# Performance work log

Measured on AMD Instinct MI355X. Metric: run time of the kernel, lower is better.

## Reference

```python
import jax, jax.numpy as jnp
import numpy as np

V = 50000      # vocab_size
E = 512        # embed_size
H = 512        # hidden_size
B = 128        # batch
S = 256        # encoder seq len
MAX_OOVS = 12


def setup_inputs() -> dict:
    key = jax.random.key(0)
    ks = jax.random.split(key, 18)
    s = 0.05
    embed_table = jax.random.normal(ks[4], (V, E), jnp.float32) * s
    embed_table = embed_table.at[0].set(0.0)  # padding_idx=0
    return {
        'input_idx':   jax.random.randint(ks[0], (B,), 0, V),
        'encoded':     jax.random.normal(ks[1], (B, S, H), jnp.float32),
        'encoded_idx': jax.random.randint(ks[2], (B, S), 0, V),
        'prev_state':  jax.random.normal(ks[3], (B, H), jnp.float32),
        'weighted':    jnp.zeros((B, 1, H), jnp.float32),
        'embed_table': embed_table,
        'Ws_w':    jax.random.normal(ks[5], (H, H), jnp.float32) * s,
        'Ws_b':    jnp.zeros((H,), jnp.float32),
        'gru_Wih': jax.random.normal(ks[6], (3 * H, E + H), jnp.float32) * s,
        'gru_Whh': jax.random.normal(ks[7], (3 * H, H), jnp.float32) * s,
        'gru_bih': jnp.zeros((3 * H,), jnp.float32),
        'gru_bhh': jnp.zeros((3 * H,), jnp.float32),
        'attn_W':  jax.random.normal(ks[8], (H, 2 * H), jnp.float32) * s,
        'attn_b':  jnp.zeros((H,), jnp.float32),
        'attn_v':  jax.random.normal(ks[9], (H,), jnp.float32) * s,
        'Wo_w':    jax.random.normal(ks[10], (V, 2 * H), jnp.float32) * s,
        'Wo_b':    jnp.zeros((V,), jnp.float32),
        'Wc_w':    jax.random.normal(ks[11], (2 * H, H), jnp.float32) * s,
        'Wc_b':    jnp.zeros((2 * H,), jnp.float32),
    }


def copy_decoder_fwd(input_idx, encoded, encoded_idx, prev_state, weighted,
                     embed_table, Ws_w, Ws_b, gru_Wih, gru_Whh, gru_bih, gru_bhh,
                     attn_W, attn_b, attn_v, Wo_w, Wo_b, Wc_w, Wc_b):
    b, seq, hidden = encoded.shape
    vocab = Wo_w.shape[0]
    dt = encoded.dtype

    # order == 0 branch: project prev_state, zero the weighted context
    prev = prev_state @ Ws_w.T + Ws_b                      # (b, h)
    wtd = jnp.zeros((b, hidden), dt)                       # (b, h)

    # GRU single step (PyTorch gate layout: r, z, n)
    x = jnp.concatenate([embed_table[input_idx], wtd], axis=1)  # (b, e+h)
    gi = x @ gru_Wih.T + gru_bih                           # (b, 3h)
    gh = prev @ gru_Whh.T + gru_bhh                        # (b, 3h)
    i_r, i_z, i_n = jnp.split(gi, 3, axis=1)
    h_r, h_z, h_n = jnp.split(gh, 3, axis=1)
    r = jax.nn.sigmoid(i_r + h_r)
    z = jax.nn.sigmoid(i_z + h_z)
    n = jnp.tanh(i_n + r * h_n)
    state = (1.0 - z) * n + z * prev                       # (b, h), == rnn_output

    # 'concat' attention: softmax_seq(v . tanh(W[h; enc] + b))
    h_exp = jnp.broadcast_to(state[:, None, :], (b, seq, hidden))
    energy = jnp.tanh(jnp.concatenate([h_exp, encoded], axis=-1) @ attn_W.T + attn_b)
    attn_w = jax.nn.softmax(energy @ attn_v, axis=1)       # (b, seq)
    context = jnp.einsum('bs,bsh->bh', attn_w, encoded)    # (b, h)

    # generation scores
    score_g = jnp.concatenate([state, context], axis=1) @ Wo_w.T + Wo_b  # (b, V)

    # copy scores
    sc = jnp.tanh(encoded @ Wc_w.T + Wc_b)                 # (b, seq, 2h)
    score_c = jnp.einsum('bsk,bk->bs', sc, jnp.concatenate([state, context], axis=1))
    score_c = score_c + jnp.where(encoded_idx == 0, -1000.0, 0.0).astype(dt)

    # joint softmax over vocab + seq
    probs = jax.nn.softmax(jnp.concatenate([score_g, score_c], axis=1), axis=1)
    prob_g = probs[:, :vocab]                              # (b, V)
    prob_c = probs[:, vocab:]                              # (b, seq)
    prob_c_given = prob_c / jnp.sum(prob_c)                # global-scalar normalization (faithful)

    # pad generation probs with small oov mass
    vext = vocab + MAX_OOVS
    prob_g_ext = jnp.concatenate(
        [prob_g, jnp.full((b, MAX_OOVS), 1e-4, dt)], axis=1)  # (b, V+oov)

    # copy -> vocab scatter-add (replaces dense one-hot + bmm)
    batch_ids = jnp.broadcast_to(jnp.arange(b)[:, None], (b, seq))
    prob_c_to_g = jnp.zeros((b, vext), dt).at[batch_ids, encoded_idx].add(prob_c)

    out = (prob_g_ext + prob_c_to_g)[:, None, :]           # (b, 1, V+oov)

    # positions in source equal to the current input token
    ind = (encoded_idx == input_idx[:, None]).astype(dt)   # (b, seq)
    ssum = ind.sum(axis=1, keepdims=True)
    ind = jnp.where(ssum > 1.0, ind / ssum, ind)
    attn2 = prob_c_given * ind                             # (b, seq)
    weighted_new = jnp.einsum('bs,bsh->bh', attn2, encoded)[:, None, :]  # (b, 1, h)

    return out, state, weighted_new


def reference(input_idx, encoded, encoded_idx, prev_state, weighted,
              embed_table, Ws_w, Ws_b, gru_Wih, gru_Whh, gru_bih, gru_bhh,
              attn_W, attn_b, attn_v, Wo_w, Wo_b, Wc_w, Wc_b):
    return copy_decoder_fwd(input_idx, encoded, encoded_idx, prev_state, weighted,
                            embed_table, Ws_w, Ws_b, gru_Wih, gru_Whh, gru_bih, gru_bhh,
                            attn_W, attn_b, attn_v, Wo_w, Wo_b, Wc_w, Wc_b)
```

## Files before the change

kernel.cpp:

```cpp
#include <hip/hip_runtime.h>
#include <hip/hip_bf16.h>
#include <math.h>

#define BB 128
#define SS 256
#define HH 512
#define VV 50000
#define VEXT 50012
#define NBLK 782
#define PST 784

typedef __bf16 bf16x8 __attribute__((ext_vector_type(8)));
typedef float f32x4 __attribute__((ext_vector_type(4)));

__device__ __forceinline__ float fast_tanh(float x) {
  float e = __expf(2.0f * x);
  return 1.0f - 2.0f / (e + 1.0f);
}
__device__ __forceinline__ float fast_sigmoid(float x) {
  return 1.0f / (1.0f + __expf(-x));
}
__device__ __forceinline__ bf16x8 cvt8(const float* p) {
  float4 a = *(const float4*)p;
  float4 b = *(const float4*)(p + 4);
  bf16x8 r;
  r[0] = (__bf16)a.x; r[1] = (__bf16)a.y; r[2] = (__bf16)a.z; r[3] = (__bf16)a.w;
  r[4] = (__bf16)b.x; r[5] = (__bf16)b.y; r[6] = (__bf16)b.z; r[7] = (__bf16)b.w;
  return r;
}

__device__ __forceinline__ void gload_lds16(const bf16x8* g, bf16x8* l) {
  __builtin_amdgcn_global_load_lds((const __attribute__((address_space(1))) void*)g,
                                   (__attribute__((address_space(3))) void*)l, 16, 0, 0);
}

__global__ void k_pack_all(const float* __restrict__ Wc_w, const float* __restrict__ attn_W,
                           const float* __restrict__ enc,
                           __hip_bfloat16* __restrict__ wc_bf,
                           __hip_bfloat16* __restrict__ wa_bf,
                           __hip_bfloat16* __restrict__ epk,
                           float* __restrict__ pc_total) {
  int i = blockIdx.x * 256 + threadIdx.x;
  if (blockIdx.x == 0 && threadIdx.x == 0) pc_total[0] = 0.f;
  if (i < 65536) {
    int l = i & 63, ks = (i >> 6) & 15, tile = i >> 10;
    int m = l & 15, q = l >> 4;
    const float* p = Wc_w + (size_t)(tile * 16 + m) * 512 + ks * 32 + q * 8;
    *(bf16x8*)(wc_bf + (size_t)i * 8) = cvt8(p);
  } else if (i < 98304) {
    int j = i - 65536;
    int l = j & 63, ks = (j >> 6) & 15, tile = j >> 10;
    int m = l & 15, q = l >> 4;
    const float* p = attn_W + (size_t)(tile * 16 + m) * 1024 + 512 + ks * 32 + q * 8;
    *(bf16x8*)(wa_bf + (size_t)j * 8) = cvt8(p);
  } else if (i < 98304 + 2097152) {
    int j = i - 98304;
    int l = j & 63, ks = (j >> 6) & 15, st = (j >> 10) & 15, b = j >> 14;
    int m = l & 15, q = l >> 4;
    const float* p = enc + ((size_t)b * SS + st * 16 + m) * HH + ks * 32 + q * 8;
    *(bf16x8*)(epk + (size_t)j * 8) = cvt8(p);
  }
}

template <int LDB, bool GATHER>
__global__ __launch_bounds__(256, 2) void k_gemm_bt(
    const float* __restrict__ A, const float* __restrict__ B,
    const float* __restrict__ bias, float* __restrict__ C, int ldc,
    const int* __restrict__ gidx) {
  __shared__ __hip_bfloat16 ylds[128 * 72];
  const int t = threadIdx.x;
  const int l = t & 63, w = t >> 6;
  const int m = l & 15, q = l >> 4;
  const int n = blockIdx.x * 64 + w * 16 + m;
  const float* wrow = B + (size_t)n * LDB;
  f32x4 acc[8];
#pragma unroll
  for (int mt = 0; mt < 8; ++mt) acc[mt] = (f32x4){0.f, 0.f, 0.f, 0.f};

  for (int kt = 0; kt < 512; kt += 64) {
    __syncthreads();
#pragma unroll
    for (int i = 0; i < 8; ++i) {
      int f = t + i * 256;
      int row = f >> 4, c4 = f & 15;
      const float* arow;
      if (GATHER)
        arow = A + (size_t)gidx[row] * 512;
      else
        arow = A + (size_t)row * 512;
      float4 v = *(const float4*)(arow + kt + c4 * 4);
      __hip_bfloat16* d = ylds + row * 72 + c4 * 4;
      d[0] = __float2bfloat16(v.x); d[1] = __float2bfloat16(v.y);
      d[2] = __float2bfloat16(v.z); d[3] = __float2bfloat16(v.w);
    }
    __syncthreads();
#pragma unroll
    for (int ksl = 0; ksl < 2; ++ksl) {
      bf16x8 bfr = cvt8(wrow + kt + ksl * 32 + q * 8);
#pragma unroll
      for (int mt = 0; mt < 8; ++mt) {
        bf16x8 af = *(const bf16x8*)(ylds + (mt * 16 + m) * 72 + ksl * 32 + q * 8);
        acc[mt] = __builtin_amdgcn_mfma_f32_16x16x32_bf16(af, bfr, acc[mt], 0, 0, 0);
      }
    }
  }
  float bv = bias[n];
#pragma unroll
  for (int mt = 0; mt < 8; ++mt) {
#pragma unroll
    for (int r = 0; r < 4; ++r) {
      int rowm = mt * 16 + q * 4 + r;
      C[(size_t)rowm * ldc + n] = acc[mt][r] + bv;
    }
  }
}

__global__ __launch_bounds__(256, 2) void k_gemm_dual(
    const float* __restrict__ A0, const float* __restrict__ B0,
    const float* __restrict__ b0, float* __restrict__ C0, int ldb0, int ldc0, int nb0,
    const float* __restrict__ A1, const float* __restrict__ B1,
    const float* __restrict__ b1, float* __restrict__ C1, int ldb1, int ldc1,
    const int* __restrict__ gidx1) {
  __shared__ __hip_bfloat16 ylds[128 * 72];
  const float* A; const float* Bw; const float* bias; float* C;
  int ldb, ldc, blk; const int* gidx;
  if ((int)blockIdx.x < nb0) {
    A = A0; Bw = B0; bias = b0; C = C0; ldb = ldb0; ldc = ldc0; gidx = nullptr; blk = blockIdx.x;
  } else {
    A = A1; Bw = B1; bias = b1; C = C1; ldb = ldb1; ldc = ldc1; gidx = gidx1; blk = blockIdx.x - nb0;
  }
  const int t = threadIdx.x;
  const int l = t & 63, w = t >> 6;
  const int m = l & 15, q = l >> 4;
  const int n = blk * 64 + w * 16 + m;
  const float* wrow = Bw + (size_t)n * ldb;
  f32x4 acc[8];
#pragma unroll
  for (int mt = 0; mt < 8; ++mt) acc[mt] = (f32x4){0.f, 0.f, 0.f, 0.f};

  for (int kt = 0; kt < 512; kt += 64) {
    __syncthreads();
#pragma unroll
    for (int i = 0; i < 8; ++i) {
      int f = t + i * 256;
      int row = f >> 4, c4 = f & 15;
      const float* arow = gidx ? (A + (size_t)gidx[row] * 512) : (A + (size_t)row * 512);
      float4 v = *(const float4*)(arow + kt + c4 * 4);
      __hip_bfloat16* d = ylds + row * 72 + c4 * 4;
      d[0] = __float2bfloat16(v.x); d[1] = __float2bfloat16(v.y);
      d[2] = __float2bfloat16(v.z); d[3] = __float2bfloat16(v.w);
    }
    __syncthreads();
#pragma unroll
    for (int ksl = 0; ksl < 2; ++ksl) {
      bf16x8 bfr = cvt8(wrow + kt + ksl * 32 + q * 8);
#pragma unroll
      for (int mt = 0; mt < 8; ++mt) {
        bf16x8 af = *(const bf16x8*)(ylds + (mt * 16 + m) * 72 + ksl * 32 + q * 8);
        acc[mt] = __builtin_amdgcn_mfma_f32_16x16x32_bf16(af, bfr, acc[mt], 0, 0, 0);
      }
    }
  }
  float bv = bias[n];
#pragma unroll
  for (int mt = 0; mt < 8; ++mt) {
#pragma unroll
    for (int r = 0; r < 4; ++r) {
      int rowm = mt * 16 + q * 4 + r;
      C[(size_t)rowm * ldc + n] = acc[mt][r] + bv;
    }
  }
}

__global__ void k_gates(const float* __restrict__ gi, const float* __restrict__ gh,
                        const float* __restrict__ prevv, float* __restrict__ state,
                        float* __restrict__ state_out) {
  int i = blockIdx.x * 256 + threadIdx.x;
  int b = i >> 9, h = i & 511;
  const float* gib = gi + (size_t)b * 1536;
  const float* ghb = gh + (size_t)b * 1536;
  float ir = gib[h], iz = gib[512 + h], inn = gib[1024 + h];
  float hr = ghb[h], hz = ghb[512 + h], hn = ghb[1024 + h];
  float r = fast_sigmoid(ir + hr);
  float z = fast_sigmoid(iz + hz);
  float n = fast_tanh(inn + r * hn);
  float st = (1.f - z) * n + z * prevv[i];
  state[i] = st;
  state_out[i] = st;
}

template <int NTOT, int MODE>
__global__ __launch_bounds__(256, 2) void k_fused3(
    const __hip_bfloat16* __restrict__ epack, const __hip_bfloat16* __restrict__ wpk,
    const float* __restrict__ biasA, const float* __restrict__ multA,
    const int* __restrict__ enc_idx, float* __restrict__ out) {
  const int b = blockIdx.x, t = threadIdx.x;
  const int l = t & 63, w = t >> 6;
  const int m = l & 15, q = l >> 4;
  const int st = blockIdx.y * 4 + w;
  __shared__ bf16x8 wbuf[2][2048];
  __shared__ float bias_l[NTOT];
  __shared__ float mult_l[NTOT];
  const float* bias_base = (MODE == 0) ? biasA + (size_t)b * HH : biasA;
  const float* mult_base = (MODE == 0) ? multA : multA + (size_t)b * 1024;
  for (int i = t; i < NTOT; i += 256) {
    bias_l[i] = bias_base[i];
    mult_l[i] = mult_base[i];
  }
  const __hip_bfloat16* ep = epack + ((size_t)(b * 16 + st) * 16) * 512 + (size_t)l * 8;
  bf16x8 afr[16];
#pragma unroll
  for (int ks = 0; ks < 16; ++ks) afr[ks] = *(const bf16x8*)(ep + ks * 512);

  const bf16x8* wv = (const bf16x8*)wpk;
  constexpr int NITER = NTOT / 32;
#pragma unroll
  for (int i = 0; i < 8; ++i)
    gload_lds16(wv + w * 64 + i * 256 + l, &wbuf[0][w * 64 + i * 256]);
  __syncthreads();

  float part[4] = {0.f, 0.f, 0.f, 0.f};
  int cur = 0;
  for (int it = 0; it < NITER; ++it) {
    if (it + 1 < NITER) {
      const bf16x8* src = wv + (size_t)(it + 1) * 2048;
#pragma unroll
      for (int i = 0; i < 8; ++i)
        gload_lds16(src + w * 64 + i * 256 + l, &wbuf[cur ^ 1][w * 64 + i * 256]);
    }
    const int nb = it * 32;
#pragma unroll
    for (int nt = 0; nt < 2; ++nt) {
      const __hip_bfloat16* wbase = (const __hip_bfloat16*)&wbuf[cur][0] + nt * 8192 + (size_t)l * 8;
      f32x4 a0 = {0.f, 0.f, 0.f, 0.f}, a1 = a0, a2 = a0, a3 = a0;
#pragma unroll
      for (int j = 0; j < 4; ++j) {
        a0 = __builtin_amdgcn_mfma_f32_16x16x32_bf16(afr[j], *(const bf16x8*)(wbase + j * 512), a0, 0, 0, 0);
        a1 = __builtin_amdgcn_mfma_f32_16x16x32_bf16(afr[4 + j], *(const bf16x8*)(wbase + (4 + j) * 512), a1, 0, 0, 0);
        a2 = __builtin_amdgcn_mfma_f32_16x16x32_bf16(afr[8 + j], *(const bf16x8*)(wbase + (8 + j) * 512), a2, 0, 0, 0);
        a3 = __builtin_amdgcn_mfma_f32_16x16x32_bf16(afr[12 + j], *(const bf16x8*)(wbase + (12 + j) * 512), a3, 0, 0, 0);
      }
      f32x4 acc = (a0 + a1) + (a2 + a3);
      const int n = nb + nt * 16 + m;
      float bias = bias_l[n];
      float mul = mult_l[n];
#pragma unroll
      for (int r = 0; r < 4; ++r) part[r] += fast_tanh(acc[r] + bias) * mul;
    }
    __syncthreads();
    cur ^= 1;
  }
#pragma unroll
  for (int r = 0; r < 4; ++r) {
    part[r] += __shfl_xor(part[r], 1, 64);
    part[r] += __shfl_xor(part[r], 2, 64);
    part[r] += __shfl_xor(part[r], 4, 64);
    part[r] += __shfl_xor(part[r], 8, 64);
  }
  if (m == 0) {
#pragma unroll
    for (int r = 0; r < 4; ++r) {
      int s = st * 16 + q * 4 + r;
      float v = part[r];
      if (MODE == 1 && enc_idx[b * SS + s] == 0) v -= 1000.0f;
      out[b * SS + s] = v;
    }
  }
}

__global__ __launch_bounds__(256, 4) void k_score_g2(
    const __hip_bfloat16* __restrict__ ypk, const float* __restrict__ Wo_w,
    const float* __restrict__ Wo_b, float* __restrict__ sg,
    float* __restrict__ ppmax, float* __restrict__ ppsum) {
  const int t = threadIdx.x;
  const int l = t & 63, w = t >> 6;
  const int m = l & 15, q = l >> 4;
  const int blk = blockIdx.x;
  const int n = blk * 64 + w * 16 + m;
  const int n_ld = (n < VV) ? n : (VV - 1);
  const float* wrow = Wo_w + (size_t)n_ld * 1024;
  f32x4 acc[8];
#pragma unroll
  for (int mt = 0; mt < 8; ++mt) acc[mt] = (f32x4){0.f, 0.f, 0.f, 0.f};

  for (int ks = 0; ks < 32; ++ks) {
    bf16x8 bfr = cvt8(wrow + ks * 32 + q * 8);
#pragma unroll
    for (int mt = 0; mt < 8; ++mt) {
      bf16x8 af = *(const bf16x8*)(ypk + (((size_t)mt * 32 + ks) * 64 + l) * 8);
      acc[mt] = __builtin_amdgcn_mfma_f32_16x16x32_bf16(af, bfr, acc[mt], 0, 0, 0);
    }
  }

  float bv = (n < VV) ? Wo_b[n] : 0.f;
#pragma unroll
  for (int mt = 0; mt < 8; ++mt) {
#pragma unroll
    for (int r = 0; r < 4; ++r) {
      float v = acc[mt][r] + bv;
      if (n < VV)
        sg[(size_t)(mt * 16 + q * 4 + r) * VV + n] = v;
      else
        v = -1e30f;
      acc[mt][r] = v;
    }
  }

  __shared__ float redA[4][128];
  __shared__ float MS[128];
#pragma unroll
  for (int mt = 0; mt < 8; ++mt) {
#pragma unroll
    for (int r = 0; r < 4; ++r) {
      float mx = acc[mt][r];
      mx = fmaxf(mx, __shfl_xor(mx, 1, 64));
      mx = fmaxf(mx, __shfl_xor(mx, 2, 64));
      mx = fmaxf(mx, __shfl_xor(mx, 4, 64));
      mx = fmaxf(mx, __shfl_xor(mx, 8, 64));
      if (m == 0) redA[w][mt * 16 + q * 4 + r] = mx;
    }
  }
  __syncthreads();
  if (t < 128)
    MS[t] = fmaxf(fmaxf(redA[0][t], redA[1][t]), fmaxf(redA[2][t], redA[3][t]));
  __syncthreads();
#pragma unroll
  for (int mt = 0; mt < 8; ++mt) {
#pragma unroll
    for (int r = 0; r < 4; ++r) {
      float s = __expf(acc[mt][r] - MS[mt * 16 + q * 4 + r]);
      s += __shfl_xor(s, 1, 64);
      s += __shfl_xor(s, 2, 64);
      s += __shfl_xor(s, 4, 64);
      s += __shfl_xor(s, 8, 64);
      if (m == 0) redA[w][mt * 16 + q * 4 + r] = s;
    }
  }
  __syncthreads();
  if (t < 128) {
    ppmax[(size_t)t * PST + blk] = MS[t];
    ppsum[(size_t)t * PST + blk] = redA[0][t] + redA[1][t] + redA[2][t] + redA[3][t];
  }
}

__global__ void k_merge(const float* __restrict__ ppmax, const float* __restrict__ ppsum,
                        const float* __restrict__ sc,
                        float* __restrict__ rmax, float* __restrict__ rsum,
                        float* __restrict__ prob_c, float* __restrict__ pc_total) {
  const int row = blockIdx.x, t = threadIdx.x;
  __shared__ float rb[8];
  __shared__ float MS[2];
  float x_sc = sc[row * SS + t];
  float mrow = x_sc;
  for (int i = t; i < NBLK; i += 256) mrow = fmaxf(mrow, ppmax[(size_t)row * PST + i]);
  for (int off = 32; off > 0; off >>= 1) mrow = fmaxf(mrow, __shfl_xor(mrow, off, 64));
  if ((t & 63) == 0) rb[t >> 6] = mrow;
  __syncthreads();
  if (t == 0) MS[0] = fmaxf(fmaxf(rb[0], rb[1]), fmaxf(rb[2], rb[3]));
  __syncthreads();
  float M = MS[0];
  float e_sc = __expf(x_sc - M);
  float s = e_sc;
  for (int i = t; i < NBLK; i += 256)
    s += ppsum[(size_t)row * PST + i] * __expf(ppmax[(size_t)row * PST + i] - M);
  for (int off = 32; off > 0; off >>= 1) s += __shfl_xor(s, off, 64);
  if ((t & 63) == 0) rb[4 + (t >> 6)] = s;
  __syncthreads();
  if (t == 0) MS[1] = rb[4] + rb[5] + rb[6] + rb[7];
  __syncthreads();
  float S = MS[1];
  if (t == 0) {
    rmax[row] = M;
    rsum[row] = S;
  }
  float pc = e_sc / S;
  prob_c[row * SS + t] = pc;
  float ps = pc;
  for (int off = 32; off > 0; off >>= 1) ps += __shfl_xor(ps, off, 64);
  if ((t & 63) == 0) rb[t >> 6] = ps;
  __syncthreads();
  if (t == 0) atomicAdd(pc_total, rb[0] + rb[1] + rb[2] + rb[3]);
}

__global__ void k_ctx(const float* __restrict__ score, const float* __restrict__ enc,
                      const float* __restrict__ state, float* __restrict__ y,
                      __hip_bfloat16* __restrict__ ypk) {
  const int b = blockIdx.x, hc = blockIdx.y, t = threadIdx.x;
  __shared__ float aws[SS];
  __shared__ float rb[4];
  float x0 = score[b * SS + t], x1 = score[b * SS + t + 128];
  float mx = fmaxf(x0, x1);
  for (int off = 32; off > 0; off >>= 1) mx = fmaxf(mx, __shfl_xor(mx, off, 64));
  if ((t & 63) == 0) rb[t >> 6] = mx;
  __syncthreads();
  mx = fmaxf(rb[0], rb[1]);
  float e0 = __expf(x0 - mx), e1 = __expf(x1 - mx);
  float s = e0 + e1;
  for (int off = 32; off > 0; off >>= 1) s += __shfl_xor(s, off, 64);
  if ((t & 63) == 0) rb[2 + (t >> 6)] = s;
  __syncthreads();
  float inv = 1.0f / (rb[2] + rb[3]);
  aws[t] = e0 * inv;
  aws[t + 128] = e1 * inv;
  __syncthreads();
  const int h = hc * 128 + t;
  float acc = 0.f;
#pragma unroll 8
  for (int ss = 0; ss < SS; ++ss) acc += aws[ss] * enc[((size_t)b * SS + ss) * HH + h];
  float sv = state[b * HH + h];
  y[(size_t)b * 1024 + h] = sv;
  y[(size_t)b * 1024 + HH + h] = acc;
  const int tile = b >> 4, mm = b & 15;
  const int c0 = h, c1 = HH + h;
  ypk[(((size_t)tile * 32 + (c0 >> 5)) * 64 + ((c0 & 31) >> 3) * 16 + mm) * 8 + (c0 & 7)] =
      __float2bfloat16(sv);
  ypk[(((size_t)tile * 32 + (c1 >> 5)) * 64 + ((c1 & 31) >> 3) * 16 + mm) * 8 + (c1 & 7)] =
      __float2bfloat16(acc);
}

__global__ void k_write_probg(const float* __restrict__ sg,
                              const float* __restrict__ rmax,
                              const float* __restrict__ rsum,
                              float* __restrict__ out) {
  int i = blockIdx.x * 256 + threadIdx.x;
  const int total = BB * VEXT;
  if (i >= total) return;
  int b = i / VEXT;
  int v = i - b * VEXT;
  float val;
  if (v < VV)
    val = __expf(sg[(size_t)b * VV + v] - rmax[b]) / rsum[b];
  else
    val = 1e-4f;
  out[i] = val;
}

__global__ void k_weighted2(const int* __restrict__ enc_idx,
                            const int* __restrict__ input_idx,
                            const float* __restrict__ prob_c,
                            const float* __restrict__ pc_total,
                            const float* __restrict__ enc,
                            float* __restrict__ wout,
                            float* __restrict__ out) {
  const int b = blockIdx.x, hc = blockIdx.y, t = threadIdx.x;
  __shared__ float f[SS];
  __shared__ float rb[2];
  const int idx_in = input_idx[b];
  const int e0i = enc_idx[b * SS + t], e1i = enc_idx[b * SS + t + 128];
  const float p0 = prob_c[b * SS + t], p1 = prob_c[b * SS + t + 128];
  if (hc == 0) {
    atomicAdd(&out[(size_t)b * VEXT + e0i], p0);
    atomicAdd(&out[(size_t)b * VEXT + e1i], p1);
  }
  int m0 = (e0i == idx_in) ? 1 : 0;
  int m1 = (e1i == idx_in) ? 1 : 0;
  float lsum = (float)(m0 + m1);
  for (int off = 32; off > 0; off >>= 1) lsum += __shfl_xor(lsum, off, 64);
  if ((t & 63) == 0) rb[t >> 6] = lsum;
  __syncthreads();
  float tot = rb[0] + rb[1];
  float norm = (tot > 1.0f) ? 1.0f / tot : 1.0f;
  float inv_pct = 1.0f / pc_total[0];
  f[t] = m0 ? p0 * inv_pct * norm : 0.f;
  f[t + 128] = m1 ? p1 * inv_pct * norm : 0.f;
  __syncthreads();
  const int h = hc * 128 + t;
  float acc = 0.f;
  for (int ss = 0; ss < SS; ++ss) acc += f[ss] * enc[((size_t)b * SS + ss) * HH + h];
  wout[b * HH + h] = acc;
}

extern "C" void kernel_launch(void* const* d_in, const int* in_sizes, int n_in,
                              void* d_out, int out_size, void* d_ws, size_t ws_size,
                              hipStream_t stream) {
  const int* input_idx = (const int*)d_in[0];
  const float* encoded = (const float*)d_in[1];
  const int* encoded_idx = (const int*)d_in[2];
  const float* prev_state = (const float*)d_in[3];
  const float* embed = (const float*)d_in[5];
  const float* Ws_w = (const float*)d_in[6];
  const float* Ws_b = (const float*)d_in[7];
  const float* gWih = (const float*)d_in[8];
  const float* gWhh = (const float*)d_in[9];
  const float* gbih = (const float*)d_in[10];
  const float* gbhh = (const float*)d_in[11];
  const float* attn_W = (const float*)d_in[12];
  const float* attn_b = (const float*)d_in[13];
  const float* attn_v = (const float*)d_in[14];
  const float* Wo_w = (const float*)d_in[15];
  const float* Wo_b = (const float*)d_in[16];
  const float* Wc_w = (const float*)d_in[17];
  const float* Wc_b = (const float*)d_in[18];

  float* out = (float*)d_out;
  float* out_state = out + (size_t)BB * VEXT;
  float* out_weighted = out_state + BB * HH;

  float* ws = (float*)d_ws;
  float* prevv = ws;
  float* state = prevv + BB * HH;
  float* hW = state + BB * HH;
  float* ascore = hW + BB * HH;
  float* aw = ascore + BB * SS;
  float* y = aw + BB * SS;
  float* sg = y + BB * 1024;
  float* sc = sg + (size_t)BB * VV;
  float* prob_c = sc + BB * SS;
  float* rmax = prob_c + BB * SS;
  float* rsum = rmax + BB;
  float* pc_total = rsum + BB;
  float* ppmax = pc_total + 64;
  float* ppsum = ppmax + (size_t)BB * PST;
  __hip_bfloat16* wc_bf = (__hip_bfloat16*)(ppsum + (size_t)BB * PST);
  __hip_bfloat16* wa_bf = wc_bf + (size_t)1024 * HH;
  __hip_bfloat16* epack = wa_bf + (size_t)512 * HH;
  __hip_bfloat16* ypk = epack + (size_t)BB * SS * HH;

  float* gi = sg;
  float* gh = sg + BB * 1536;

  k_pack_all<<<8576, 256, 0, stream>>>(Wc_w, attn_W, encoded, wc_bf, wa_bf, epack, pc_total);

  k_gemm_dual<<<32, 256, 0, stream>>>(prev_state, Ws_w, Ws_b, prevv, 512, 512, 8,
                                      embed, gWih, gbih, gi, 1024, 1536, input_idx);
  k_gemm_bt<512, false><<<24, 256, 0, stream>>>(prevv, gWhh, gbhh, gh, 1536, nullptr);
  k_gates<<<256, 256, 0, stream>>>(gi, gh, prevv, state, out_state);
  k_gemm_bt<1024, false><<<8, 256, 0, stream>>>(state, attn_W, attn_b, hW, 512, nullptr);

  k_fused3<HH, 0><<<dim3(BB, 4), 256, 0, stream>>>(epack, wa_bf, hW, attn_v,
                                                   nullptr, ascore);
  k_ctx<<<dim3(BB, 4), 128, 0, stream>>>(ascore, encoded, state, y, ypk);

  k_score_g2<<<NBLK, 256, 0, stream>>>(ypk, Wo_w, Wo_b, sg, ppmax, ppsum);
  k_fused3<1024, 1><<<dim3(BB, 4), 256, 0, stream>>>(epack, wc_bf, Wc_b, y,
                                                     encoded_idx, sc);

  k_merge<<<BB, 256, 0, stream>>>(ppmax, ppsum, sc, rmax, rsum, prob_c, pc_total);
  k_write_probg<<<(BB * VEXT + 255) / 256, 256, 0, stream>>>(sg, rmax, rsum, out);
  k_weighted2<<<dim3(BB, 4), 128, 0, stream>>>(encoded_idx, input_idx, prob_c, pc_total,
                                               encoded, out_weighted, out);
}
```

Baseline: 697.3 us.

## Split vocab-score GEMM tiles across batch halves and prefetch weight fragments

The output-projection kernel now covers 32 vocab columns per block instead of 64. Its four waves are split into two column tiles by two batch halves, so each wave keeps four accumulators instead of eight, and the launch bound allows eight blocks per CU. The kernel launches twice as many blocks, and the next k-step's Wo_w fragment is loaded while the current MFMAs run. The cost is that each weight row is now read by two waves. The partial max/sum buffers double in size, so the merge kernel reads more entries per row.

```diff
diff --git a/kernel.cpp b/kernel.cpp
--- a/kernel.cpp
+++ b/kernel.cpp
@@ -7,8 +7,8 @@
 #define HH 512
 #define VV 50000
 #define VEXT 50012
-#define NBLK 782
-#define PST 784
+#define NBLK2 1563
+#define PST 1568
 
 typedef __bf16 bf16x8 __attribute__((ext_vector_type(8)));
 typedef float f32x4 __attribute__((ext_vector_type(4)));
@@ -268,48 +268,53 @@
   }
 }
 
-__global__ __launch_bounds__(256, 4) void k_score_g2(
+__global__ __launch_bounds__(256, 8) void k_score_g3(
     const __hip_bfloat16* __restrict__ ypk, const float* __restrict__ Wo_w,
     const float* __restrict__ Wo_b, float* __restrict__ sg,
     float* __restrict__ ppmax, float* __restrict__ ppsum) {
   const int t = threadIdx.x;
   const int l = t & 63, w = t >> 6;
   const int m = l & 15, q = l >> 4;
+  const int ntile = w & 1, mhalf = w >> 1;
   const int blk = blockIdx.x;
-  const int n = blk * 64 + w * 16 + m;
+  const int n = blk * 32 + ntile * 16 + m;
   const int n_ld = (n < VV) ? n : (VV - 1);
   const float* wrow = Wo_w + (size_t)n_ld * 1024;
-  f32x4 acc[8];
-#pragma unroll
-  for (int mt = 0; mt < 8; ++mt) acc[mt] = (f32x4){0.f, 0.f, 0.f, 0.f};
-
+  const __hip_bfloat16* ybase = ypk + ((size_t)mhalf * 4 * 32 * 64 + l) * 8;
+  f32x4 acc[4];
+#pragma unroll
+  for (int mt = 0; mt < 4; ++mt) acc[mt] = (f32x4){0.f, 0.f, 0.f, 0.f};
+
+  bf16x8 bcur = cvt8(wrow + q * 8);
   for (int ks = 0; ks < 32; ++ks) {
-    bf16x8 bfr = cvt8(wrow + ks * 32 + q * 8);
-#pragma unroll
-    for (int mt = 0; mt < 8; ++mt) {
-      bf16x8 af = *(const bf16x8*)(ypk + (((size_t)mt * 32 + ks) * 64 + l) * 8);
-      acc[mt] = __builtin_amdgcn_mfma_f32_16x16x32_bf16(af, bfr, acc[mt], 0, 0, 0);
-    }
+    bf16x8 bnxt = bcur;
+    if (ks + 1 < 32) bnxt = cvt8(wrow + (ks + 1) * 32 + q * 8);
+#pragma unroll
+    for (int mt = 0; mt < 4; ++mt) {
+      bf16x8 af = *(const bf16x8*)(ybase + ((size_t)(mt * 32 + ks) * 64) * 8);
+      acc[mt] = __builtin_amdgcn_mfma_f32_16x16x32_bf16(af, bcur, acc[mt], 0, 0, 0);
+    }
+    bcur = bnxt;
   }
 
   float bv = (n < VV) ? Wo_b[n] : 0.f;
 #pragma unroll
-  for (int mt = 0; mt < 8; ++mt) {
+  for (int mt = 0; mt < 4; ++mt) {
 #pragma unroll
     for (int r = 0; r < 4; ++r) {
       float v = acc[mt][r] + bv;
       if (n < VV)
-        sg[(size_t)(mt * 16 + q * 4 + r) * VV + n] = v;
+        sg[(size_t)(mhalf * 64 + mt * 16 + q * 4 + r) * VV + n] = v;
       else
         v = -1e30f;
       acc[mt][r] = v;
     }
   }
 
-  __shared__ float redA[4][128];
+  __shared__ float redA[4][64];
   __shared__ float MS[128];
 #pragma unroll
-  for (int mt = 0; mt < 8; ++mt) {
+  for (int mt = 0; mt < 4; ++mt) {
 #pragma unroll
     for (int r = 0; r < 4; ++r) {
       float mx = acc[mt][r];
@@ -321,14 +326,16 @@
     }
   }
   __syncthreads();
-  if (t < 128)
-    MS[t] = fmaxf(fmaxf(redA[0][t], redA[1][t]), fmaxf(redA[2][t], redA[3][t]));
-  __syncthreads();
-#pragma unroll
-  for (int mt = 0; mt < 8; ++mt) {
+  if (t < 128) {
+    int mh = t >> 6, idx = t & 63;
+    MS[t] = fmaxf(redA[2 * mh][idx], redA[2 * mh + 1][idx]);
+  }
+  __syncthreads();
+#pragma unroll
+  for (int mt = 0; mt < 4; ++mt) {
 #pragma unroll
     for (int r = 0; r < 4; ++r) {
-      float s = __expf(acc[mt][r] - MS[mt * 16 + q * 4 + r]);
+      float s = __expf(acc[mt][r] - MS[mhalf * 64 + mt * 16 + q * 4 + r]);
       s += __shfl_xor(s, 1, 64);
       s += __shfl_xor(s, 2, 64);
       s += __shfl_xor(s, 4, 64);
@@ -338,8 +345,9 @@
   }
   __syncthreads();
   if (t < 128) {
+    int mh = t >> 6, idx = t & 63;
     ppmax[(size_t)t * PST + blk] = MS[t];
-    ppsum[(size_t)t * PST + blk] = redA[0][t] + redA[1][t] + redA[2][t] + redA[3][t];
+    ppsum[(size_t)t * PST + blk] = redA[2 * mh][idx] + redA[2 * mh + 1][idx];
   }
 }
 
@@ -352,7 +360,7 @@
   __shared__ float MS[2];
   float x_sc = sc[row * SS + t];
   float mrow = x_sc;
-  for (int i = t; i < NBLK; i += 256) mrow = fmaxf(mrow, ppmax[(size_t)row * PST + i]);
+  for (int i = t; i < NBLK2; i += 256) mrow = fmaxf(mrow, ppmax[(size_t)row * PST + i]);
   for (int off = 32; off > 0; off >>= 1) mrow = fmaxf(mrow, __shfl_xor(mrow, off, 64));
   if ((t & 63) == 0) rb[t >> 6] = mrow;
   __syncthreads();
@@ -361,7 +369,7 @@
   float M = MS[0];
   float e_sc = __expf(x_sc - M);
   float s = e_sc;
-  for (int i = t; i < NBLK; i += 256)
+  for (int i = t; i < NBLK2; i += 256)
     s += ppsum[(size_t)row * PST + i] * __expf(ppmax[(size_t)row * PST + i] - M);
   for (int off = 32; off > 0; off >>= 1) s += __shfl_xor(s, off, 64);
   if ((t & 63) == 0) rb[4 + (t >> 6)] = s;
@@ -531,7 +539,7 @@
                                                    nullptr, ascore);
   k_ctx<<<dim3(BB, 4), 128, 0, stream>>>(ascore, encoded, state, y, ypk);
 
-  k_score_g2<<<NBLK, 256, 0, stream>>>(ypk, Wo_w, Wo_b, sg, ppmax, ppsum);
+  k_score_g3<<<NBLK2, 256, 0, stream>>>(ypk, Wo_w, Wo_b, sg, ppmax, ppsum);
   k_fused3<1024, 1><<<dim3(BB, 4), 256, 0, stream>>>(epack, wc_bf, Wc_b, y,
                                                      encoded_idx, sc);
 
```

Result: slower. 715.4 us (+2.6%).
